# Kernel tuning notes

Hardware: AMD Instinct MI355X
Metric: run time of the kernel (lower is better)

The kernel has to match this reference:

```python
import jax, jax.numpy as jnp
import numpy as np

SIGMA = 3.0          # vdW clash radius
HB_R0 = 2.9          # ideal N..O hbond distance
HB_SIG2 = 0.2 ** 2   # hbond gaussian width^2
EPS = 1e-6


def setup_inputs() -> dict:
    key = jax.random.key(0)
    k1, k2 = jax.random.split(key)
    coords = jax.random.normal(k1, (8, 512, 4, 3), dtype=jnp.float32)
    motors = jax.random.normal(k2, (8, 512, 8), dtype=jnp.float32)
    mask = jnp.ones((8, 512), dtype=jnp.float32)
    return {"coords": coords, "motors": motors, "mask": mask}


def _energy(coords, motors, mask):
    B, S, A, _ = coords.shape
    dt = coords.dtype

    # ---- vdW repulsion over all atom pairs: [B, S*A, S*A] ----
    flat = coords.reshape(B, S * A, 3)
    fmask = jnp.repeat(mask, A, axis=1)                       # [B, S*A]
    dist_sq = jnp.sum((flat[:, :, None, :] - flat[:, None, :, :]) ** 2, axis=-1)
    r = jnp.sqrt(dist_sq + EPS)
    overlap = jnp.maximum(SIGMA - r, 0.0)
    clash = overlap ** 4
    pair_mask = fmask[:, :, None] * fmask[:, None, :]
    pair_mask = pair_mask * (1.0 - jnp.eye(S * A, dtype=dt)[None])
    lj = jnp.sum(clash * pair_mask) / (jnp.sum(pair_mask) + EPS)

    # ---- hydrogen-bond energy: N (atom 0) vs O (atom 3), [B, S, S] ----
    Nc = coords[:, :, 0, :]
    Oc = coords[:, :, 3, :]
    dist = jnp.sqrt(jnp.sum((Nc[:, :, None, :] - Oc[:, None, :, :]) ** 2, axis=-1))
    h_energy = jnp.exp(-0.5 * (dist - HB_R0) ** 2 / HB_SIG2)
    idx = jnp.arange(S)
    range_mask = (jnp.abs(idx[None, :] - idx[:, None]) > 2).astype(dt)
    pm = mask[:, :, None] * mask[:, None, :] * range_mask[None]
    hb = -jnp.sum(h_energy * pm) / (jnp.sum(mask) + EPS)

    # ---- motor smoothness ----
    diff = jnp.sum((motors[:, 1:] - motors[:, :-1]) ** 2, axis=-1)
    m_mask = mask[:, 1:] * mask[:, :-1]
    motor = jnp.sum(diff * m_mask) / (jnp.sum(m_mask) + EPS)

    # ---- radius of gyration on CA (atom 1) ----
    ca = coords[:, :, 1, :]
    msum = jnp.sum(mask, axis=1, keepdims=True)               # [B,1]
    mean_pos = jnp.sum(ca * mask[:, :, None], axis=1) / (msum + EPS)
    d2 = jnp.sum((ca - mean_pos[:, None, :]) ** 2, axis=-1)
    rg_sq = jnp.sum(d2 * mask, axis=1) / (msum[:, 0] + EPS)
    rg = jnp.mean(rg_sq)

    return 1.0 * lj + 0.5 * hb + 0.1 * motor + 0.05 * rg


def reference(coords, motors, mask):
    return _energy(coords, motors, mask)
```

## Files before the change

### kernel.cpp

```cpp
#include <hip/hip_runtime.h>
#include <hip/hip_bf16.h>
#include <math.h>

#define B 8
#define S 512
#define A 4
#define N (S*A)
#define SIGMA 3.0f
#define HB_R0 2.9f
#define HB_COEF (-12.5f)
#define EPS 1e-6f

#define NLJ 576
#define NHB 64
#define NAUX 8
#define NBLOCKS (NLJ + NHB + NAUX)

#define WS_LJ  0
#define WS_HB  576
#define WS_AUX 640

__device__ __forceinline__ float wave_reduce_sum(float v) {
    #pragma unroll
    for (int off = 32; off > 0; off >>= 1) v += __shfl_down(v, off, 64);
    return v;
}

__global__ __launch_bounds__(256) void physics_main(
        const float* __restrict__ coords,
        const float* __restrict__ motors,
        const float* __restrict__ mask,
        float* __restrict__ ws) {
    const int bid = blockIdx.x;
    const int tid = threadIdx.x;

    __shared__ float4 sj[128];
    __shared__ float  redbuf[32];

    const int wid = tid >> 6, lane = tid & 63;

    if (bid < NLJ) {
        const int b    = bid / 72;
        const int r    = bid % 72;
        const int p    = r >> 1;
        const int half = r & 1;
        int it = 0, pp = p;
        while (pp >= 8 - it) { pp -= 8 - it; ++it; }
        const int jt = it + pp;

        const float* cb = coords + (size_t)b * N * 3;
        const float* mb = mask + b * S;
        const int jlo = jt * 256 + half * 128;

        if (tid < 128) {
            const int j = jlo + tid;
            sj[tid] = make_float4(cb[j*3+0], cb[j*3+1], cb[j*3+2], mb[j >> 2]);
        }
        __syncthreads();

        const int i = it * 256 + tid;
        const float xi = cb[i*3+0], yi = cb[i*3+1], zi = cb[i*3+2];
        const float fmi = mb[i >> 2];

        float acc = 0.f;
        #pragma unroll 8
        for (int jj = 0; jj < 128; ++jj) {
            const float4 q = sj[jj];
            const float dx = xi - q.x;
            const float dy = yi - q.y;
            const float dz = zi - q.z;
            const float d2 = fmaf(dx, dx, fmaf(dy, dy, fmaf(dz, dz, EPS)));
            const float rr = __builtin_amdgcn_sqrtf(d2);
            const float ov = fmaxf(SIGMA - rr, 0.f);
            const float ov2 = ov * ov;
            acc = fmaf(ov2 * ov2, q.w, acc);
        }
        if (it == jt && i >= jlo && i < jlo + 128) {
            const float ovd = SIGMA - __builtin_amdgcn_sqrtf(EPS);
            const float o2 = ovd * ovd;
            acc -= fmi * (o2 * o2);
        }
        float v = fmi * acc;
        if (it != jt) v *= 2.f;

        v = wave_reduce_sum(v);
        if (lane == 0) redbuf[wid] = v;
        __syncthreads();
        if (tid == 0) ws[WS_LJ + bid] = redbuf[0] + redbuf[1] + redbuf[2] + redbuf[3];

    } else if (bid < NLJ + NHB) {
        const int idx = bid - NLJ;
        const int b  = idx >> 3;
        const int rr_ = idx & 7;
        const int it = rr_ >> 2;
        const int jh = rr_ & 3;

        const float* cb = coords + (size_t)b * S * A * 3;
        const float* mb = mask + b * S;
        const int jlo = jh * 128;

        if (tid < 128) {
            const int j = jlo + tid;
            sj[tid] = make_float4(cb[(j*4+3)*3+0], cb[(j*4+3)*3+1],
                                  cb[(j*4+3)*3+2], mb[j]);
        }
        __syncthreads();

        const int i = it * 256 + tid;
        const float xi = cb[(i*4+0)*3+0];
        const float yi = cb[(i*4+0)*3+1];
        const float zi = cb[(i*4+0)*3+2];
        const float mi = mb[i];

        float acc = 0.f;
        #pragma unroll 8
        for (int jj = 0; jj < 128; ++jj) {
            const float4 q = sj[jj];
            const float dx = xi - q.x;
            const float dy = yi - q.y;
            const float dz = zi - q.z;
            const float d2 = fmaf(dx, dx, fmaf(dy, dy, dz * dz));
            const float dist = __builtin_amdgcn_sqrtf(d2);
            const float t = dist - HB_R0;
            const float e = __expf(HB_COEF * (t * t));
            acc = fmaf(e, q.w, acc);
        }
        #pragma unroll
        for (int dj = -2; dj <= 2; ++dj) {
            const int j = i + dj;
            if (j >= jlo && j < jlo + 128) {
                const float4 q = sj[j - jlo];
                const float dx = xi - q.x;
                const float dy = yi - q.y;
                const float dz = zi - q.z;
                const float d2 = fmaf(dx, dx, fmaf(dy, dy, dz * dz));
                const float dist = __builtin_amdgcn_sqrtf(d2);
                const float t = dist - HB_R0;
                const float e = __expf(HB_COEF * (t * t));
                acc -= e * q.w;
            }
        }
        float v = mi * acc;
        v = wave_reduce_sum(v);
        if (lane == 0) redbuf[wid] = v;
        __syncthreads();
        if (tid == 0) ws[WS_HB + idx] = redbuf[0] + redbuf[1] + redbuf[2] + redbuf[3];

    } else {
        const int b = bid - NLJ - NHB;
        const float* cb = coords + (size_t)b * S * A * 3;
        const float* mb = mask + b * S;

        float s1x = 0.f, s1y = 0.f, s1z = 0.f, s2 = 0.f, M = 0.f, Sm2 = 0.f;
        float mn = 0.f, md = 0.f;

        for (int s = tid; s < S; s += 256) {
            const float m = mb[s];
            const float* ca = cb + ((size_t)(s*4 + 1)) * 3;
            const float x = ca[0], y = ca[1], z = ca[2];
            s1x = fmaf(x, m, s1x);
            s1y = fmaf(y, m, s1y);
            s1z = fmaf(z, m, s1z);
            s2  = fmaf(fmaf(x, x, fmaf(y, y, z * z)), m, s2);
            M   += m;
            Sm2 = fmaf(m, m, Sm2);
            if (s < S - 1) {
                const float mm = m * mb[s + 1];
                const float4* m4 = (const float4*)(motors + ((size_t)b * S + s) * 8);
                const float4 a0 = m4[0], a1 = m4[1], b0 = m4[2], b1 = m4[3];
                float d = 0.f;
                float df;
                df = b0.x - a0.x; d = fmaf(df, df, d);
                df = b0.y - a0.y; d = fmaf(df, df, d);
                df = b0.z - a0.z; d = fmaf(df, df, d);
                df = b0.w - a0.w; d = fmaf(df, df, d);
                df = b1.x - a1.x; d = fmaf(df, df, d);
                df = b1.y - a1.y; d = fmaf(df, df, d);
                df = b1.z - a1.z; d = fmaf(df, df, d);
                df = b1.w - a1.w; d = fmaf(df, df, d);
                mn = fmaf(d, mm, mn);
                md += mm;
            }
        }

        float vals[8] = {s1x, s1y, s1z, s2, M, Sm2, mn, md};
        #pragma unroll
        for (int k = 0; k < 8; ++k) {
            float v = wave_reduce_sum(vals[k]);
            if (lane == 0) redbuf[wid * 8 + k] = v;
        }
        __syncthreads();
        if (tid < 8) {
            const float t = redbuf[tid] + redbuf[8 + tid] + redbuf[16 + tid] + redbuf[24 + tid];
            ws[WS_AUX + b * 8 + tid] = t;
        }
    }
}

__global__ __launch_bounds__(256) void physics_final(
        const float* __restrict__ ws, float* __restrict__ out) {
    const int tid = threadIdx.x;
    const int wid = tid >> 6, lane = tid & 63;
    __shared__ float redbuf[8];

    float lj = 0.f;
    for (int i = tid; i < NLJ; i += 256) lj += ws[WS_LJ + i];
    float hb = (tid < NHB) ? ws[WS_HB + tid] : 0.f;

    lj = wave_reduce_sum(lj);
    hb = wave_reduce_sum(hb);
    if (lane == 0) { redbuf[wid * 2 + 0] = lj; redbuf[wid * 2 + 1] = hb; }
    __syncthreads();

    if (tid == 0) {
        const float lj_num = redbuf[0] + redbuf[2] + redbuf[4] + redbuf[6];
        const float hb_num = redbuf[1] + redbuf[3] + redbuf[5] + redbuf[7];

        float lj_den = 0.f, masksum = 0.f, mnum = 0.f, mden = 0.f, rg = 0.f;
        #pragma unroll
        for (int b = 0; b < B; ++b) {
            const float* p = ws + WS_AUX + b * 8;
            const float M = p[4], Sm2 = p[5];
            lj_den  += 16.f * M * M - 4.f * Sm2;
            masksum += M;
            mnum    += p[6];
            mden    += p[7];
            const float Me = M + EPS;
            const float mx = p[0] / Me, my = p[1] / Me, mz = p[2] / Me;
            const float d2sum = p[3] - 2.f * (mx * p[0] + my * p[1] + mz * p[2])
                              + (mx * mx + my * my + mz * mz) * M;
            rg += d2sum / Me;
        }
        rg *= (1.f / (float)B);

        const float ljv   = lj_num / (lj_den + EPS);
        const float hbv   = -hb_num / (masksum + EPS);
        const float motor = mnum / (mden + EPS);
        out[0] = ljv + 0.5f * hbv + 0.1f * motor + 0.05f * rg;
    }
}

extern "C" void kernel_launch(void* const* d_in, const int* in_sizes, int n_in,
                              void* d_out, int out_size, void* d_ws, size_t ws_size,
                              hipStream_t stream) {
    const float* coords = (const float*)d_in[0];
    const float* motors = (const float*)d_in[1];
    const float* mask   = (const float*)d_in[2];
    float* ws  = (float*)d_ws;
    float* out = (float*)d_out;

    physics_main<<<NBLOCKS, 256, 0, stream>>>(coords, motors, mask, ws);
    physics_final<<<1, 256, 0, stream>>>(ws, out);
}
```

Baseline: 70.57 us.

## Fuse final reduction via last-block ticket and read j-tiles directly from global

Merges the two kernels into one: each block bumps a global atomic ticket, and the block that draws the last ticket (modulo block count) does the final cross-block reduction and writes the output. This removes the second kernel launch. It also drops the shared-memory staging of j coordinates in the LJ and H-bond loops, so every thread reads the same j values from global or cache as a uniform broadcast load, which removes one barrier per block. The cost is extra global loads per inner iteration, and a ticket counter that persists across calls and is never reset, relying on modulo arithmetic.

```diff
diff --git a/kernel.cpp b/kernel.cpp
--- a/kernel.cpp
+++ b/kernel.cpp
@@ -1,5 +1,4 @@
 #include <hip/hip_runtime.h>
-#include <hip/hip_bf16.h>
 #include <math.h>
 
 #define B 8
@@ -20,24 +19,26 @@
 #define WS_HB  576
 #define WS_AUX 640
 
+__device__ unsigned long long g_ticket = 0ull;
+
 __device__ __forceinline__ float wave_reduce_sum(float v) {
     #pragma unroll
     for (int off = 32; off > 0; off >>= 1) v += __shfl_down(v, off, 64);
     return v;
 }
 
-__global__ __launch_bounds__(256) void physics_main(
+__global__ __launch_bounds__(256) void physics_fused(
         const float* __restrict__ coords,
         const float* __restrict__ motors,
         const float* __restrict__ mask,
-        float* __restrict__ ws) {
+        float* __restrict__ ws,
+        float* __restrict__ out) {
     const int bid = blockIdx.x;
     const int tid = threadIdx.x;
-
-    __shared__ float4 sj[128];
-    __shared__ float  redbuf[32];
-
     const int wid = tid >> 6, lane = tid & 63;
+
+    __shared__ float redbuf[32];
+    __shared__ int   slast;
 
     if (bid < NLJ) {
         const int b    = bid / 72;
@@ -51,12 +52,8 @@
         const float* cb = coords + (size_t)b * N * 3;
         const float* mb = mask + b * S;
         const int jlo = jt * 256 + half * 128;
-
-        if (tid < 128) {
-            const int j = jlo + tid;
-            sj[tid] = make_float4(cb[j*3+0], cb[j*3+1], cb[j*3+2], mb[j >> 2]);
-        }
-        __syncthreads();
+        const float* jc = cb + (size_t)jlo * 3;
+        const float* jm = mb + (jlo >> 2);
 
         const int i = it * 256 + tid;
         const float xi = cb[i*3+0], yi = cb[i*3+1], zi = cb[i*3+2];
@@ -65,15 +62,18 @@
         float acc = 0.f;
         #pragma unroll 8
         for (int jj = 0; jj < 128; ++jj) {
-            const float4 q = sj[jj];
-            const float dx = xi - q.x;
-            const float dy = yi - q.y;
-            const float dz = zi - q.z;
+            const float qx = jc[jj*3+0];
+            const float qy = jc[jj*3+1];
+            const float qz = jc[jj*3+2];
+            const float qw = jm[jj >> 2];
+            const float dx = xi - qx;
+            const float dy = yi - qy;
+            const float dz = zi - qz;
             const float d2 = fmaf(dx, dx, fmaf(dy, dy, fmaf(dz, dz, EPS)));
             const float rr = __builtin_amdgcn_sqrtf(d2);
             const float ov = fmaxf(SIGMA - rr, 0.f);
             const float ov2 = ov * ov;
-            acc = fmaf(ov2 * ov2, q.w, acc);
+            acc = fmaf(ov2 * ov2, qw, acc);
         }
         if (it == jt && i >= jlo && i < jlo + 128) {
             const float ovd = SIGMA - __builtin_amdgcn_sqrtf(EPS);
@@ -91,20 +91,13 @@
     } else if (bid < NLJ + NHB) {
         const int idx = bid - NLJ;
         const int b  = idx >> 3;
-        const int rr_ = idx & 7;
-        const int it = rr_ >> 2;
-        const int jh = rr_ & 3;
+        const int r8 = idx & 7;
+        const int it = r8 >> 2;
+        const int jh = r8 & 3;
 
         const float* cb = coords + (size_t)b * S * A * 3;
         const float* mb = mask + b * S;
         const int jlo = jh * 128;
-
-        if (tid < 128) {
-            const int j = jlo + tid;
-            sj[tid] = make_float4(cb[(j*4+3)*3+0], cb[(j*4+3)*3+1],
-                                  cb[(j*4+3)*3+2], mb[j]);
-        }
-        __syncthreads();
 
         const int i = it * 256 + tid;
         const float xi = cb[(i*4+0)*3+0];
@@ -115,29 +108,35 @@
         float acc = 0.f;
         #pragma unroll 8
         for (int jj = 0; jj < 128; ++jj) {
-            const float4 q = sj[jj];
-            const float dx = xi - q.x;
-            const float dy = yi - q.y;
-            const float dz = zi - q.z;
+            const int j = jlo + jj;
+            const float qx = cb[(j*4+3)*3+0];
+            const float qy = cb[(j*4+3)*3+1];
+            const float qz = cb[(j*4+3)*3+2];
+            const float qw = mb[j];
+            const float dx = xi - qx;
+            const float dy = yi - qy;
+            const float dz = zi - qz;
             const float d2 = fmaf(dx, dx, fmaf(dy, dy, dz * dz));
             const float dist = __builtin_amdgcn_sqrtf(d2);
             const float t = dist - HB_R0;
             const float e = __expf(HB_COEF * (t * t));
-            acc = fmaf(e, q.w, acc);
+            acc = fmaf(e, qw, acc);
         }
         #pragma unroll
         for (int dj = -2; dj <= 2; ++dj) {
             const int j = i + dj;
             if (j >= jlo && j < jlo + 128) {
-                const float4 q = sj[j - jlo];
-                const float dx = xi - q.x;
-                const float dy = yi - q.y;
-                const float dz = zi - q.z;
+                const float qx = cb[(j*4+3)*3+0];
+                const float qy = cb[(j*4+3)*3+1];
+                const float qz = cb[(j*4+3)*3+2];
+                const float dx = xi - qx;
+                const float dy = yi - qy;
+                const float dz = zi - qz;
                 const float d2 = fmaf(dx, dx, fmaf(dy, dy, dz * dz));
                 const float dist = __builtin_amdgcn_sqrtf(d2);
                 const float t = dist - HB_R0;
                 const float e = __expf(HB_COEF * (t * t));
-                acc -= e * q.w;
+                acc -= e * mb[j];
             }
         }
         float v = mi * acc;
@@ -195,48 +194,51 @@
             ws[WS_AUX + b * 8 + tid] = t;
         }
     }
-}
-
-__global__ __launch_bounds__(256) void physics_final(
-        const float* __restrict__ ws, float* __restrict__ out) {
-    const int tid = threadIdx.x;
-    const int wid = tid >> 6, lane = tid & 63;
-    __shared__ float redbuf[8];
-
-    float lj = 0.f;
-    for (int i = tid; i < NLJ; i += 256) lj += ws[WS_LJ + i];
-    float hb = (tid < NHB) ? ws[WS_HB + tid] : 0.f;
-
-    lj = wave_reduce_sum(lj);
-    hb = wave_reduce_sum(hb);
-    if (lane == 0) { redbuf[wid * 2 + 0] = lj; redbuf[wid * 2 + 1] = hb; }
+
     __syncthreads();
-
     if (tid == 0) {
-        const float lj_num = redbuf[0] + redbuf[2] + redbuf[4] + redbuf[6];
-        const float hb_num = redbuf[1] + redbuf[3] + redbuf[5] + redbuf[7];
-
-        float lj_den = 0.f, masksum = 0.f, mnum = 0.f, mden = 0.f, rg = 0.f;
-        #pragma unroll
-        for (int b = 0; b < B; ++b) {
-            const float* p = ws + WS_AUX + b * 8;
-            const float M = p[4], Sm2 = p[5];
-            lj_den  += 16.f * M * M - 4.f * Sm2;
-            masksum += M;
-            mnum    += p[6];
-            mden    += p[7];
-            const float Me = M + EPS;
-            const float mx = p[0] / Me, my = p[1] / Me, mz = p[2] / Me;
-            const float d2sum = p[3] - 2.f * (mx * p[0] + my * p[1] + mz * p[2])
-                              + (mx * mx + my * my + mz * mz) * M;
-            rg += d2sum / Me;
-        }
-        rg *= (1.f / (float)B);
-
-        const float ljv   = lj_num / (lj_den + EPS);
-        const float hbv   = -hb_num / (masksum + EPS);
-        const float motor = mnum / (mden + EPS);
-        out[0] = ljv + 0.5f * hbv + 0.1f * motor + 0.05f * rg;
+        __threadfence();
+        const unsigned long long t = atomicAdd(&g_ticket, 1ull);
+        slast = ((int)(t % (unsigned long long)NBLOCKS) == NBLOCKS - 1) ? 1 : 0;
+    }
+    __syncthreads();
+    if (slast) {
+        __threadfence();
+        float lj = 0.f;
+        for (int k = tid; k < NLJ; k += 256) lj += ws[WS_LJ + k];
+        float hb = (tid < NHB) ? ws[WS_HB + tid] : 0.f;
+
+        lj = wave_reduce_sum(lj);
+        hb = wave_reduce_sum(hb);
+        if (lane == 0) { redbuf[wid * 2 + 0] = lj; redbuf[wid * 2 + 1] = hb; }
+        __syncthreads();
+
+        if (tid == 0) {
+            const float lj_num = redbuf[0] + redbuf[2] + redbuf[4] + redbuf[6];
+            const float hb_num = redbuf[1] + redbuf[3] + redbuf[5] + redbuf[7];
+
+            float lj_den = 0.f, masksum = 0.f, mnum = 0.f, mden = 0.f, rg = 0.f;
+            #pragma unroll
+            for (int b = 0; b < B; ++b) {
+                const float* p = ws + WS_AUX + b * 8;
+                const float M = p[4], Sm2 = p[5];
+                lj_den  += 16.f * M * M - 4.f * Sm2;
+                masksum += M;
+                mnum    += p[6];
+                mden    += p[7];
+                const float Me = M + EPS;
+                const float mx = p[0] / Me, my = p[1] / Me, mz = p[2] / Me;
+                const float d2sum = p[3] - 2.f * (mx * p[0] + my * p[1] + mz * p[2])
+                                  + (mx * mx + my * my + mz * mz) * M;
+                rg += d2sum / Me;
+            }
+            rg *= (1.f / (float)B);
+
+            const float ljv   = lj_num / (lj_den + EPS);
+            const float hbv   = -hb_num / (masksum + EPS);
+            const float motor = mnum / (mden + EPS);
+            out[0] = ljv + 0.5f * hbv + 0.1f * motor + 0.05f * rg;
+        }
     }
 }
 
@@ -249,6 +251,5 @@
     float* ws  = (float*)d_ws;
     float* out = (float*)d_out;
 
-    physics_main<<<NBLOCKS, 256, 0, stream>>>(coords, motors, mask, ws);
-    physics_final<<<1, 256, 0, stream>>>(ws, out);
+    physics_fused<<<NBLOCKS, 256, 0, stream>>>(coords, motors, mask, ws, out);
 }
```

After: 80.50 us. 14.1% more time.
